# Optimization experiments

Measured on AMD Instinct MI355X. Metric: run time of the kernel, lower is better.

The kernel has to match this reference:

```python
import jax, jax.numpy as jnp
import numpy as np

BLOCK = 64
# Standard NF4 codebook (bitsandbytes), 16 quantile-based values in [-1, 1].
NF4_CODEBOOK = jnp.array([
    -1.0, -0.6961928009986877, -0.5250730514526367, -0.39491748809814453,
    -0.28444138169288635, -0.18477343022823334, -0.09105003625154495, 0.0,
    0.07958029955625534, 0.16093020141124725, 0.24611230194568634,
    0.33791524171829224, 0.44070982933044434, 0.5626170039176941,
    0.6848514676094055, 1.0], dtype=jnp.float32)


def dequantize_nf4(codes, absmax, shape):
    # codes: int array of 4-bit indices (unpacked), absmax: one scale per BLOCK.
    vals = NF4_CODEBOOK[codes.reshape(-1)]              # [N]
    vals = vals.reshape(-1, BLOCK) * absmax[:, None]    # blockwise rescale
    return vals.reshape(shape)


def setup_inputs() -> dict:
    key = jax.random.key(0)
    k1, k2, k3, k4, k5 = jax.random.split(key, 5)
    B, S, D_IN, D_OUT = 4, 2048, 4096, 4096
    x = jax.random.normal(k1, (B, S, D_IN), dtype=jnp.float32)
    w_codes = jax.random.randint(k2, (D_OUT, D_IN), 0, 16, dtype=jnp.int32)
    w_absmax = jax.random.uniform(k3, (D_OUT * D_IN // BLOCK,), dtype=jnp.float32)
    b_codes = jax.random.randint(k4, (D_OUT,), 0, 16, dtype=jnp.int32)
    b_absmax = jax.random.uniform(k5, (D_OUT // BLOCK,), dtype=jnp.float32)
    return {"x": x, "w_codes": w_codes, "w_absmax": w_absmax,
            "b_codes": b_codes, "b_absmax": b_absmax}


def reference(x, w_codes, w_absmax, b_codes, b_absmax):
    W = dequantize_nf4(w_codes, w_absmax, w_codes.shape)   # [out, in]
    b = dequantize_nf4(b_codes, b_absmax, b_codes.shape)   # [out]
    # F.linear(x, W, b) = x @ W.T + b
    return jnp.einsum('bsd,od->bso', x, W) + b
```

## Files before the change

### kernel.cpp

```cpp
#include <hip/hip_runtime.h>
#include <stdint.h>

typedef __bf16 bf16_t;
typedef __attribute__((ext_vector_type(8))) __bf16 bf16x8;
typedef __attribute__((ext_vector_type(4))) float f32x4;
typedef __attribute__((ext_vector_type(8))) unsigned short ushort8;
typedef __attribute__((ext_vector_type(4))) unsigned short us4;
typedef __attribute__((ext_vector_type(4))) int int4v;
typedef __attribute__((ext_vector_type(4))) float float4v;

typedef const void __attribute__((address_space(1)))* gptr_t;
typedef void __attribute__((address_space(3)))* lptr_t;

__constant__ float NF4_CB[16] = {
    -1.0f, -0.6961928009986877f, -0.5250730514526367f, -0.39491748809814453f,
    -0.28444138169288635f, -0.18477343022823334f, -0.09105003625154495f, 0.0f,
    0.07958029955625534f, 0.16093020141124725f, 0.24611230194568634f,
    0.33791524171829224f, 0.44070982933044434f, 0.5626170039176941f,
    0.6848514676094055f, 1.0f};

__device__ __forceinline__ unsigned short f32_to_bf16_rne(float f) {
    unsigned int u = __float_as_uint(f);
    u += 0x7FFFu + ((u >> 16) & 1u);
    return (unsigned short)(u >> 16);
}

__global__ __launch_bounds__(256) void prep_kernel2(
        const int* __restrict__ w_codes, const float* __restrict__ w_absmax,
        const float* __restrict__ x,
        const int* __restrict__ b_codes, const float* __restrict__ b_absmax,
        unsigned short* __restrict__ outW, unsigned short* __restrict__ outA,
        float* __restrict__ outBias,
        long nW4, long nX4, long nBias) {
    __shared__ float cb[16];
    if (threadIdx.x < 16) cb[threadIdx.x] = NF4_CB[threadIdx.x];
    __syncthreads();

    const long total = nW4 + nX4 + nBias;
    const long stride = (long)gridDim.x * blockDim.x;
    for (long u = (long)blockIdx.x * blockDim.x + threadIdx.x; u < total;
         u += stride) {
        if (u < nW4) {
            int4v c = *(const int4v*)(w_codes + u * 4);
            float am = w_absmax[u >> 4];
            us4 v;
            v[0] = f32_to_bf16_rne(cb[c[0]] * am);
            v[1] = f32_to_bf16_rne(cb[c[1]] * am);
            v[2] = f32_to_bf16_rne(cb[c[2]] * am);
            v[3] = f32_to_bf16_rne(cb[c[3]] * am);
            *(us4*)(outW + u * 4) = v;
        } else if (u < nW4 + nX4) {
            long i = u - nW4;
            float4v f = *(const float4v*)(x + i * 4);
            us4 v;
            v[0] = f32_to_bf16_rne(f[0]);
            v[1] = f32_to_bf16_rne(f[1]);
            v[2] = f32_to_bf16_rne(f[2]);
            v[3] = f32_to_bf16_rne(f[3]);
            *(us4*)(outA + i * 4) = v;
        } else {
            long o = u - nW4 - nX4;
            outBias[o] = cb[b_codes[o]] * b_absmax[o >> 6];
        }
    }
}

__global__ __launch_bounds__(512) void gemm_bias_kernel_256(
        const bf16_t* __restrict__ A, const bf16_t* __restrict__ B,
        const float* __restrict__ bias, float* __restrict__ C,
        int M, int N, int K) {
    __shared__ __align__(16) bf16_t sAB[24576];

    const int t = threadIdx.x;
    const int lane = t & 63;
    const int wave = t >> 6;
    const int tileM = blockIdx.y * 256;
    const int tileN = blockIdx.x * 128;

    const int rloc = lane >> 3;
    const int jsw  = (lane & 7) ^ rloc;
    const bf16_t* srcp[6];
    bf16_t* dstp[6];
#pragma unroll
    for (int j = 0; j < 6; ++j) {
        int c = wave * 6 + j;
        int isB = (c >= 32);
        int r = (isB ? (c - 32) : c) * 8 + rloc;
        const bf16_t* base = isB ? (B + (size_t)(tileN + r) * K)
                                 : (A + (size_t)(tileM + r) * K);
        srcp[j] = base + jsw * 8;
        dstp[j] = &sAB[c * 512 + lane * 8];
    }

    const int wm = wave >> 1;
    const int wn = wave & 1;
    const int la = lane & 15;
    const int jA = lane >> 4;
    const int jj0 = (jA ^ (lane & 7)) * 8;
    const int aoff = (wm * 64 + la) * 64 + jj0;
    const int boff = 16384 + (wn * 64 + la) * 64 + jj0;

    f32x4 acc[4][4] = {};

    for (int kt = 0; kt < K; kt += 64) {
#pragma unroll
        for (int j = 0; j < 6; ++j) {
            __builtin_amdgcn_global_load_lds((gptr_t)(srcp[j]), (lptr_t)(dstp[j]),
                                             16, 0, 0);
            srcp[j] += 64;
        }
        __syncthreads();

#pragma unroll
        for (int kh = 0; kh < 2; ++kh) {
            const int kx = kh * 32;
            bf16x8 a[4], b[4];
#pragma unroll
            for (int i = 0; i < 4; ++i) a[i] = *(const bf16x8*)&sAB[(aoff + i * 1024) ^ kx];
#pragma unroll
            for (int i = 0; i < 4; ++i) b[i] = *(const bf16x8*)&sAB[(boff + i * 1024) ^ kx];
#pragma unroll
            for (int mi = 0; mi < 4; ++mi)
#pragma unroll
                for (int ni = 0; ni < 4; ++ni)
                    acc[mi][ni] = __builtin_amdgcn_mfma_f32_16x16x32_bf16(
                        a[mi], b[ni], acc[mi][ni], 0, 0, 0);
        }
        __syncthreads();
    }

    const int col0 = tileN + wn * 64 + la;
    const int row0 = tileM + wm * 64 + jA * 4;
    float bv[4];
#pragma unroll
    for (int ni = 0; ni < 4; ++ni) bv[ni] = bias[col0 + ni * 16];
#pragma unroll
    for (int mi = 0; mi < 4; ++mi)
#pragma unroll
        for (int ni = 0; ni < 4; ++ni)
#pragma unroll
            for (int r = 0; r < 4; ++r)
                C[(size_t)(row0 + mi * 16 + r) * N + (col0 + ni * 16)] =
                    acc[mi][ni][r] + bv[ni];
}

__global__ void gemm_bias_kernel_128(const bf16_t* __restrict__ A,
                                     const bf16_t* __restrict__ B,
                                     const float* __restrict__ bias,
                                     float* __restrict__ C,
                                     int M, int N, int K) {
    __shared__ __align__(16) bf16_t sAB[16384];
    const int t = threadIdx.x;
    const int lane = t & 63;
    const int wave = t >> 6;
    const int tileM = blockIdx.y * 128;
    const int tileN = blockIdx.x * 128;

    const int rloc = lane >> 3;
    const int jsw  = (lane & 7) ^ rloc;
    const int chunk0 = wave * 8;
    const int isB = chunk0 >> 4;
    const int ci0 = chunk0 & 15;
    const int r0 = ci0 * 8 + rloc;
    const bf16_t* srcp = (isB ? (B + (size_t)(tileN + r0) * K)
                              : (A + (size_t)(tileM + r0) * K)) + jsw * 8;
    bf16_t* dstp = &sAB[isB * 8192 + ci0 * 512 + lane * 8];
    const size_t srcChunkStride = (size_t)8 * K;

    const int wm = wave >> 1;
    const int wn = wave & 1;
    const int la = lane & 15;
    const int jA = lane >> 4;
    const int jj0 = (jA ^ (lane & 7)) * 8;
    const int aoff = (wm * 64 + la) * 64 + jj0;
    const int boff = 8192 + (wn * 64 + la) * 64 + jj0;

    f32x4 acc[4][4] = {};
    for (int kt = 0; kt < K; kt += 64) {
#pragma unroll
        for (int j8 = 0; j8 < 8; ++j8)
            __builtin_amdgcn_global_load_lds((gptr_t)(srcp + j8 * srcChunkStride),
                                             (lptr_t)(dstp + j8 * 512), 16, 0, 0);
        srcp += 64;
        __syncthreads();
#pragma unroll
        for (int kh = 0; kh < 2; ++kh) {
            const int kx = kh * 32;
            bf16x8 a[4], b[4];
#pragma unroll
            for (int i = 0; i < 4; ++i) a[i] = *(const bf16x8*)&sAB[(aoff + i * 1024) ^ kx];
#pragma unroll
            for (int i = 0; i < 4; ++i) b[i] = *(const bf16x8*)&sAB[(boff + i * 1024) ^ kx];
#pragma unroll
            for (int mi = 0; mi < 4; ++mi)
#pragma unroll
                for (int ni = 0; ni < 4; ++ni)
                    acc[mi][ni] = __builtin_amdgcn_mfma_f32_16x16x32_bf16(
                        a[mi], b[ni], acc[mi][ni], 0, 0, 0);
        }
        __syncthreads();
    }
    const int col0 = tileN + wn * 64 + la;
    const int row0 = tileM + wm * 64 + jA * 4;
    float bv[4];
#pragma unroll
    for (int ni = 0; ni < 4; ++ni) bv[ni] = bias[col0 + ni * 16];
#pragma unroll
    for (int mi = 0; mi < 4; ++mi)
#pragma unroll
        for (int ni = 0; ni < 4; ++ni)
#pragma unroll
            for (int r = 0; r < 4; ++r)
                C[(size_t)(row0 + mi * 16 + r) * N + (col0 + ni * 16)] =
                    acc[mi][ni][r] + bv[ni];
}

extern "C" void kernel_launch(void* const* d_in, const int* in_sizes, int n_in,
                              void* d_out, int out_size, void* d_ws, size_t ws_size,
                              hipStream_t stream) {
    const float* x        = (const float*)d_in[0];
    const int*   w_codes  = (const int*)d_in[1];
    const float* w_absmax = (const float*)d_in[2];
    const int*   b_codes  = (const int*)d_in[3];
    const float* b_absmax = (const float*)d_in[4];
    float* out = (float*)d_out;

    const int  D_OUT = in_sizes[3];
    const long WK    = (long)in_sizes[1];
    const int  D_IN  = (int)(WK / D_OUT);
    const long xN    = (long)in_sizes[0];
    const int  M     = (int)(xN / D_IN);
    const int  N = D_OUT, K = D_IN;

    unsigned short* wsW = (unsigned short*)d_ws;
    unsigned short* wsA = wsW + (size_t)N * K;
    float* wsBias = (float*)(wsA + (size_t)M * K);

    long nW4 = WK / 4;
    long nX4 = xN / 4;
    long nBias = D_OUT;
    long totalUnits = nW4 + nX4 + nBias;
    long nblk = (totalUnits + 255) / 256;
    if (nblk > 2048) nblk = 2048;

    for (int rep = 0; rep < 3; ++rep) {
        prep_kernel2<<<dim3((unsigned)nblk), dim3(256), 0, stream>>>(
            w_codes, w_absmax, x, b_codes, b_absmax, wsW, wsA, wsBias,
            nW4, nX4, nBias);
    }

    if (M % 256 == 0) {
        gemm_bias_kernel_256<<<dim3(N / 128, M / 256), dim3(512), 0, stream>>>(
            (const bf16_t*)wsA, (const bf16_t*)wsW, wsBias, out, M, N, K);
    } else {
        gemm_bias_kernel_128<<<dim3(N / 128, M / 128), dim3(256), 0, stream>>>(
            (const bf16_t*)wsA, (const bf16_t*)wsW, wsBias, out, M, N, K);
    }
}
```

Measured before the change: 604.5 us.

## Add 256x256 phased bf16 MFMA GEMM with XCD-aware tile remap, drop repeated prep launches

Adds a new GEMM kernel with 256x256 output tiles, double-buffered LDS filled by direct global-to-LDS loads, and a four-phase loop that interleaves staging, LDS reads and MFMA groups between barriers. It uses setprio around the MFMA groups and remaps workgroup IDs across eight groups for better cache locality. It also removes the redundant triple launch of the prep kernel so dequantization runs once. The larger tile raises reuse per loaded byte but uses 128KB of LDS and many accumulator registers, which limits occupancy.

```diff
diff --git a/kernel.cpp b/kernel.cpp
--- a/kernel.cpp
+++ b/kernel.cpp
@@ -4,7 +4,6 @@
 typedef __bf16 bf16_t;
 typedef __attribute__((ext_vector_type(8))) __bf16 bf16x8;
 typedef __attribute__((ext_vector_type(4))) float f32x4;
-typedef __attribute__((ext_vector_type(8))) unsigned short ushort8;
 typedef __attribute__((ext_vector_type(4))) unsigned short us4;
 typedef __attribute__((ext_vector_type(4))) int int4v;
 typedef __attribute__((ext_vector_type(4))) float float4v;
@@ -65,6 +64,134 @@
     }
 }
 
+#define FENCE() asm volatile("" ::: "memory")
+#define BAR() do { FENCE(); __builtin_amdgcn_s_barrier(); FENCE(); } while (0)
+
+#define READ_A(dst, H, KH, BASE) do { \
+  _Pragma("unroll") for (int i_ = 0; i_ < 4; ++i_) \
+    dst[i_] = *(const bf16x8*)&sAB[((aoff + (4*(H) + i_) * 1024) ^ ((KH) << 5)) + (BASE)]; \
+} while (0)
+
+#define READ_B(dst, KH, BASE) do { \
+  _Pragma("unroll") for (int i_ = 0; i_ < 4; ++i_) \
+    dst[i_] = *(const bf16x8*)&sAB[((boff + i_ * 1024) ^ ((KH) << 5)) + (BASE)]; \
+} while (0)
+
+#define MFMA16(areg, breg, H) do { \
+  __builtin_amdgcn_s_setprio(1); \
+  _Pragma("unroll") for (int mi_ = 0; mi_ < 4; ++mi_) \
+    _Pragma("unroll") for (int ni_ = 0; ni_ < 4; ++ni_) \
+      acc[4*(H) + mi_][ni_] = __builtin_amdgcn_mfma_f32_16x16x32_bf16( \
+          areg[mi_], breg[ni_], acc[4*(H) + mi_][ni_], 0, 0, 0); \
+  __builtin_amdgcn_s_setprio(0); \
+} while (0)
+
+#define STAGE4(J0, SDST) do { \
+  _Pragma("unroll") for (int j_ = 0; j_ < 4; ++j_) { \
+    __builtin_amdgcn_global_load_lds((gptr_t)srcp[(J0) + j_], \
+        (lptr_t)((SDST) + ((J0) + j_) * 512), 16, 0, 0); \
+    srcp[(J0) + j_] += 64; \
+  } \
+} while (0)
+
+__global__ __launch_bounds__(512, 2) void gemm_bias_kernel_256x256_ph(
+        const bf16_t* __restrict__ A, const bf16_t* __restrict__ B,
+        const float* __restrict__ bias, float* __restrict__ C,
+        int M, int N, int K) {
+    __shared__ __align__(16) bf16_t sAB[65536];
+
+    const int t = threadIdx.x;
+    const int lane = t & 63;
+    const int wave = t >> 6;
+
+    const int nbx = gridDim.x;
+    const int nwg = nbx * (int)gridDim.y;
+    int flat = (int)blockIdx.y * nbx + (int)blockIdx.x;
+    if ((nwg & 7) == 0) flat = (flat & 7) * (nwg >> 3) + (flat >> 3);
+    const int tileM = (flat / nbx) * 256;
+    const int tileN = (flat % nbx) * 256;
+
+    const int rloc = lane >> 3;
+    const int jsw  = (lane & 7) ^ rloc;
+    const bf16_t* srcp[8];
+#pragma unroll
+    for (int j = 0; j < 8; ++j) {
+        int c = wave * 8 + j;
+        int isB = c >> 5;
+        int r = (c & 31) * 8 + rloc;
+        const bf16_t* base = isB ? (B + (size_t)(tileN + r) * K)
+                                 : (A + (size_t)(tileM + r) * K);
+        srcp[j] = base + jsw * 8;
+    }
+    bf16_t* dst0 = &sAB[wave * 4096 + lane * 8];
+
+    const int wm = wave >> 2;
+    const int wn = wave & 3;
+    const int la = lane & 15;
+    const int jA = lane >> 4;
+    const int jj0 = (jA ^ (lane & 7)) * 8;
+    const int aoff = (wm * 128 + la) * 64 + jj0;
+    const int boff = 16384 + (wn * 64 + la) * 64 + jj0;
+
+    f32x4 acc[8][4] = {};
+    const int nt = K >> 6;
+
+#pragma unroll
+    for (int j = 0; j < 8; ++j) {
+        __builtin_amdgcn_global_load_lds((gptr_t)srcp[j], (lptr_t)(dst0 + j * 512),
+                                         16, 0, 0);
+        srcp[j] += 64;
+    }
+    asm volatile("s_waitcnt vmcnt(0)" ::: "memory");
+    BAR();
+
+    for (int kt = 0; kt < nt; ++kt) {
+        const int base = (kt & 1) << 15;
+        bf16_t* sdst = dst0 + ((((kt & 1) ^ 1)) << 15);
+        const bool st = (kt + 1 < nt);
+        bf16x8 a[4], b0[4], b1[4];
+
+        if (st) STAGE4(0, sdst);
+        READ_A(a, 0, 0, base);
+        READ_B(b0, 0, base);
+        BAR();
+        MFMA16(a, b0, 0);
+        BAR();
+
+        if (st) STAGE4(4, sdst);
+        READ_A(a, 1, 0, base);
+        BAR();
+        MFMA16(a, b0, 1);
+        BAR();
+
+        READ_A(a, 1, 1, base);
+        READ_B(b1, 1, base);
+        BAR();
+        MFMA16(a, b1, 1);
+        BAR();
+
+        READ_A(a, 0, 1, base);
+        BAR();
+        MFMA16(a, b1, 0);
+        asm volatile("s_waitcnt vmcnt(0)" ::: "memory");
+        BAR();
+    }
+
+    const int col0 = tileN + wn * 64 + la;
+    const int row0 = tileM + wm * 128 + jA * 4;
+    float bv[4];
+#pragma unroll
+    for (int ni = 0; ni < 4; ++ni) bv[ni] = bias[col0 + ni * 16];
+#pragma unroll
+    for (int mi = 0; mi < 8; ++mi)
+#pragma unroll
+        for (int ni = 0; ni < 4; ++ni)
+#pragma unroll
+            for (int r = 0; r < 4; ++r)
+                C[(size_t)(row0 + mi * 16 + r) * N + (col0 + ni * 16)] =
+                    acc[mi][ni][r] + bv[ni];
+}
+
 __global__ __launch_bounds__(512) void gemm_bias_kernel_256(
         const bf16_t* __restrict__ A, const bf16_t* __restrict__ B,
         const float* __restrict__ bias, float* __restrict__ C,
@@ -242,14 +369,14 @@
     long totalUnits = nW4 + nX4 + nBias;
     long nblk = (totalUnits + 255) / 256;
     if (nblk > 2048) nblk = 2048;
-
-    for (int rep = 0; rep < 3; ++rep) {
-        prep_kernel2<<<dim3((unsigned)nblk), dim3(256), 0, stream>>>(
-            w_codes, w_absmax, x, b_codes, b_absmax, wsW, wsA, wsBias,
-            nW4, nX4, nBias);
-    }
-
-    if (M % 256 == 0) {
+    prep_kernel2<<<dim3((unsigned)nblk), dim3(256), 0, stream>>>(
+        w_codes, w_absmax, x, b_codes, b_absmax, wsW, wsA, wsBias,
+        nW4, nX4, nBias);
+
+    if (M % 256 == 0 && N % 256 == 0 && K % 64 == 0) {
+        gemm_bias_kernel_256x256_ph<<<dim3(N / 256, M / 256), dim3(512), 0, stream>>>(
+            (const bf16_t*)wsA, (const bf16_t*)wsW, wsBias, out, M, N, K);
+    } else if (M % 256 == 0) {
         gemm_bias_kernel_256<<<dim3(N / 128, M / 256), dim3(512), 0, stream>>>(
             (const bf16_t*)wsA, (const bf16_t*)wsW, wsBias, out, M, N, K);
     } else {
```

Measured after the change: 492.3 us. 1.23x faster.
